# Performance work log

Hardware: AMD Instinct MI355X
Metric: run time of the kernel (lower is better)

Reference implementation:

```python
import jax, jax.numpy as jnp
import numpy as np

B, NB, S, D = 4096, 16, 256, 1024


def setup_inputs() -> dict:
    key = jax.random.key(0)
    k = jax.random.split(key, 6)
    sc_in = 1.0 / np.sqrt(D)
    sc_out = 1.0 / np.sqrt(S)
    return {
        "x": jax.random.normal(k[0], (B, D), dtype=jnp.float32),
        "y_index": jax.random.randint(k[1], (B, 1), 0, NB, dtype=jnp.int64),
        "W_in": jax.random.uniform(k[2], (NB, S, D), jnp.float32, -sc_in, sc_in),
        "b_in": jax.random.uniform(k[3], (NB, S), jnp.float32, -sc_in, sc_in),
        "W_out": jax.random.uniform(k[4], (NB, D, S), jnp.float32, -sc_out, sc_out),
        "b_out": jax.random.uniform(k[5], (NB, D), jnp.float32, -sc_out, sc_out),
    }


def reference(x, y_index, W_in, b_in, W_out, b_out):
    # h: [B, D] -> relu applied before every branch's fc_in (as in torch source)
    h = jax.nn.relu(x)
    # hiddens for all branches: [B, NB, S]
    hid = jnp.einsum("bd,nsd->bns", h, W_in) + b_in[None, :, :]
    # branch outputs stacked: [B, NB, D]
    outs = jnp.einsum("bns,nds->bnd", hid, W_out) + b_out[None, :, :]
    # gather selected branch per token: [B, D]
    sel = jnp.take_along_axis(outs, y_index[:, :, None], axis=1)[:, 0, :]
    return x + sel
```

## Files before the change

### kernel.cpp

```cpp
#include <hip/hip_runtime.h>


typedef unsigned short u16;
typedef short bf16x8 __attribute__((ext_vector_type(8)));
typedef float f32x4 __attribute__((ext_vector_type(4)));

#define MFMA16 __builtin_amdgcn_mfma_f32_16x16x32_bf16

constexpr int B_TOK = 4096;
constexpr int NB = 16;
constexpr int S_DIM = 256;
constexpr int D_DIM = 1024;
constexpr int BM = 64;
constexpr int PAD_ROWS = B_TOK + NB * BM;
constexpr int NTILES = PAD_ROWS / BM;

__device__ __forceinline__ unsigned short f2bf(float f) {
    unsigned u = __builtin_bit_cast(unsigned, f);
    u += 0x7fffu + ((u >> 16) & 1u);
    return (unsigned short)(u >> 16);
}
__device__ __forceinline__ unsigned pack2(float a, float b) {
    return (unsigned)f2bf(a) | ((unsigned)f2bf(b) << 16);
}
__device__ __forceinline__ void gload_lds16(const void* g, void* l) {
    __builtin_amdgcn_global_load_lds(
        (const __attribute__((address_space(1))) void*)g,
        (__attribute__((address_space(3))) void*)l, 16, 0, 0);
}
__device__ __forceinline__ void publish() {
    asm volatile("s_waitcnt vmcnt(0)" ::: "memory");
    __syncthreads();
}

__global__ __launch_bounds__(256) void prep_kernel(
    const float* __restrict__ Wi_f, const float* __restrict__ Wo_f,
    u16* __restrict__ Wi, u16* __restrict__ Wo,
    const int* __restrict__ y, int* __restrict__ perm, int* __restrict__ tileBranch) {
    const int t = threadIdx.x;
    if (blockIdx.x == 0) {
        __shared__ int hist[NB];
        __shared__ int aoff[NB + 1];
        __shared__ int cursor[NB];
        if (t < NB) hist[t] = 0;
        __syncthreads();
        for (int i = t; i < B_TOK; i += 256) atomicAdd(&hist[y[i]], 1);
        __syncthreads();
        if (t == 0) {
            int off = 0;
            for (int n = 0; n < NB; ++n) {
                aoff[n] = off;
                cursor[n] = off;
                off += ((hist[n] + BM - 1) / BM) * BM;
            }
            aoff[NB] = off;
        }
        __syncthreads();
        for (int i = t; i < NTILES; i += 256) {
            int rb = i * BM, br = -1;
            for (int n = 0; n < NB; ++n)
                if (rb >= aoff[n] && rb < aoff[n + 1]) br = n;
            tileBranch[i] = br;
        }
        for (int i = t; i < PAD_ROWS; i += 256) perm[i] = -1;
        __syncthreads();
        for (int i = t; i < B_TOK; i += 256) {
            int pos = atomicAdd(&cursor[y[i]], 1);
            perm[pos] = i;
        }
        return;
    }
    int i = (blockIdx.x - 1) * 256 + t;
    const float* src;
    u16* dst;
    int j;
    if (i < 524288) { src = Wi_f; dst = Wi; j = i; }
    else            { src = Wo_f; dst = Wo; j = i - 524288; }
    const float4* p = (const float4*)src + (size_t)j * 2;
    float4 v0 = p[0], v1 = p[1];
    uint4 o;
    o.x = pack2(v0.x, v0.y);
    o.y = pack2(v0.z, v0.w);
    o.z = pack2(v1.x, v1.y);
    o.w = pack2(v1.z, v1.w);
    ((uint4*)dst)[j] = o;
}

__global__ __launch_bounds__(256) void gemm1_kernel(
    const float* __restrict__ x, const u16* __restrict__ Wi,
    const float* __restrict__ b_in, const int* __restrict__ tileBranch,
    const int* __restrict__ perm, u16* __restrict__ Hp) {
    const int branch = tileBranch[blockIdx.y];
    if (branch < 0) return;
    const int rowBase = blockIdx.y * BM;
    const int colBase = blockIdx.x * 64;

    __shared__ u16 sA[2][64 * 64];
    __shared__ u16 sB[2][64 * 64];

    const int t = threadIdx.x;
    const int ar = t >> 2;
    const int acg = t & 3;
    const int tok = perm[rowBase + ar];
    const float* aSrc = (tok >= 0) ? (x + (size_t)tok * D_DIM + acg * 16) : x;
    const int abyte0 = (ar * 128 + acg * 32) ^ ((ar & 7) << 4);
    const int abyte1 = abyte0 ^ 16;

    const u16* Bb = Wi + (size_t)branch * S_DIM * D_DIM + (size_t)colBase * D_DIM;

    const int lane = t & 63;
    const int wid = t >> 6;
    const int wm = (wid >> 1) * 32;
    const int wn = (wid & 1) * 32;
    const int fr = lane & 15;
    const int kc = (lane >> 4) << 3;

    f32x4 acc[2][2] = {};

    auto stageB = [&](int buf, int k0) {
#pragma unroll
        for (int i = 0; i < 2; ++i) {
            const int L = i * 4096 + t * 16;
            const int row = L >> 7;
            const int sunit = ((L >> 4) & 7) ^ (row & 7);
            gload_lds16((const char*)Bb + (size_t)row * (D_DIM * 2) + k0 * 2 + sunit * 16,
                        (char*)sB[buf] + L);
        }
    };
    auto packWriteA = [&](int buf, float4 v0, float4 v1, float4 v2, float4 v3) {
        uint4 w0, w1;
        if (tok >= 0) {
            w0.x = pack2(fmaxf(v0.x, 0.f), fmaxf(v0.y, 0.f));
            w0.y = pack2(fmaxf(v0.z, 0.f), fmaxf(v0.w, 0.f));
            w0.z = pack2(fmaxf(v1.x, 0.f), fmaxf(v1.y, 0.f));
            w0.w = pack2(fmaxf(v1.z, 0.f), fmaxf(v1.w, 0.f));
            w1.x = pack2(fmaxf(v2.x, 0.f), fmaxf(v2.y, 0.f));
            w1.y = pack2(fmaxf(v2.z, 0.f), fmaxf(v2.w, 0.f));
            w1.z = pack2(fmaxf(v3.x, 0.f), fmaxf(v3.y, 0.f));
            w1.w = pack2(fmaxf(v3.z, 0.f), fmaxf(v3.w, 0.f));
        } else {
            w0 = make_uint4(0, 0, 0, 0);
            w1 = make_uint4(0, 0, 0, 0);
        }
        *(uint4*)((char*)sA[buf] + abyte0) = w0;
        *(uint4*)((char*)sA[buf] + abyte1) = w1;
    };

    float4 v0, v1, v2, v3;
    {
        const float4* p = (const float4*)aSrc;
        v0 = p[0]; v1 = p[1]; v2 = p[2]; v3 = p[3];
    }
    stageB(0, 0);
    packWriteA(0, v0, v1, v2, v3);
    publish();

    for (int kt = 0; kt < 16; ++kt) {
        const int cur = kt & 1;
        if (kt < 15) {
            const int k0n = (kt + 1) << 6;
            stageB(cur ^ 1, k0n);
            const float4* p = (const float4*)(aSrc + k0n);
            v0 = p[0]; v1 = p[1]; v2 = p[2]; v3 = p[3];
        }
#pragma unroll
        for (int kk = 0; kk < 2; ++kk) {
            const int kcol = kc + kk * 32;
            const int ra0 = wm + fr, ra1 = wm + 16 + fr;
            const int rb0 = wn + fr, rb1 = wn + 16 + fr;
            bf16x8 a0 = *(const bf16x8*)&sA[cur][(ra0 * 64 + kcol) ^ ((ra0 & 7) << 3)];
            bf16x8 a1 = *(const bf16x8*)&sA[cur][(ra1 * 64 + kcol) ^ ((ra1 & 7) << 3)];
            bf16x8 b0 = *(const bf16x8*)&sB[cur][(rb0 * 64 + kcol) ^ ((rb0 & 7) << 3)];
            bf16x8 b1 = *(const bf16x8*)&sB[cur][(rb1 * 64 + kcol) ^ ((rb1 & 7) << 3)];
            acc[0][0] = MFMA16(a0, b0, acc[0][0], 0, 0, 0);
            acc[0][1] = MFMA16(a0, b1, acc[0][1], 0, 0, 0);
            acc[1][0] = MFMA16(a1, b0, acc[1][0], 0, 0, 0);
            acc[1][1] = MFMA16(a1, b1, acc[1][1], 0, 0, 0);
        }
        if (kt < 15) packWriteA(cur ^ 1, v0, v1, v2, v3);
        publish();
    }

    const int r0 = (lane >> 4) * 4;
#pragma unroll
    for (int m = 0; m < 2; ++m) {
        const int prow0 = rowBase + wm + m * 16 + r0;
#pragma unroll
        for (int n = 0; n < 2; ++n) {
            const int col = colBase + wn + n * 16 + fr;
            const float bv = b_in[branch * S_DIM + col];
#pragma unroll
            for (int r = 0; r < 4; ++r)
                Hp[(size_t)(prow0 + r) * S_DIM + col] = f2bf(acc[m][n][r] + bv);
        }
    }
}

__global__ __launch_bounds__(256) void gemm2_kernel(
    const u16* __restrict__ Hp, const u16* __restrict__ Wo,
    const float* __restrict__ b_out, const int* __restrict__ tileBranch,
    const int* __restrict__ perm, const float* __restrict__ x,
    float* __restrict__ out) {
    const int branch = tileBranch[blockIdx.y];
    if (branch < 0) return;
    const int rowBase = blockIdx.y * BM;
    const int colBase = blockIdx.x * 128;

    __shared__ __align__(16) char smem[49152];
    u16* sA0 = (u16*)smem;
    u16* sA1 = (u16*)(smem + 8192);
    u16* sB0 = (u16*)(smem + 16384);
    u16* sB1 = (u16*)(smem + 32768);

    const int t = threadIdx.x;
    const u16* Ab = Hp + (size_t)rowBase * S_DIM;
    const u16* Bb = Wo + (size_t)branch * D_DIM * S_DIM + (size_t)colBase * S_DIM;

    const int lane = t & 63;
    const int wid = t >> 6;
    const int wm = (wid >> 1) * 32;
    const int wn = (wid & 1) * 64;
    const int fr = lane & 15;
    const int kc = (lane >> 4) << 3;

    f32x4 acc[2][4] = {};

    auto stage = [&](u16* dA, u16* dB, int k0) {
#pragma unroll
        for (int i = 0; i < 2; ++i) {
            const int L = i * 4096 + t * 16;
            const int row = L >> 7;
            const int sunit = ((L >> 4) & 7) ^ (row & 7);
            gload_lds16((const char*)Ab + (size_t)row * (S_DIM * 2) + k0 * 2 + sunit * 16,
                        (char*)dA + L);
        }
#pragma unroll
        for (int i = 0; i < 4; ++i) {
            const int L = i * 4096 + t * 16;
            const int row = L >> 7;
            const int sunit = ((L >> 4) & 7) ^ (row & 7);
            gload_lds16((const char*)Bb + (size_t)row * (S_DIM * 2) + k0 * 2 + sunit * 16,
                        (char*)dB + L);
        }
    };
    auto compute = [&](const u16* cA, const u16* cB) {
#pragma unroll
        for (int kk = 0; kk < 2; ++kk) {
            const int kcol = kc + kk * 32;
            const int ra0 = wm + fr, ra1 = wm + 16 + fr;
            bf16x8 a0 = *(const bf16x8*)&cA[(ra0 * 64 + kcol) ^ ((ra0 & 7) << 3)];
            bf16x8 a1 = *(const bf16x8*)&cA[(ra1 * 64 + kcol) ^ ((ra1 & 7) << 3)];
            bf16x8 b[4];
#pragma unroll
            for (int n = 0; n < 4; ++n) {
                const int rb = wn + n * 16 + fr;
                b[n] = *(const bf16x8*)&cB[(rb * 64 + kcol) ^ ((rb & 7) << 3)];
            }
#pragma unroll
            for (int n = 0; n < 4; ++n) {
                acc[0][n] = MFMA16(a0, b[n], acc[0][n], 0, 0, 0);
                acc[1][n] = MFMA16(a1, b[n], acc[1][n], 0, 0, 0);
            }
        }
    };

    stage(sA0, sB0, 0);
    publish();
#pragma unroll
    for (int kt = 0; kt < 4; ++kt) {
        const bool even = (kt & 1) == 0;
        if (kt < 3) stage(even ? sA1 : sA0, even ? sB1 : sB0, (kt + 1) << 6);
        compute(even ? sA0 : sA1, even ? sB0 : sB1);
        publish();
    }

    float* bo = (float*)smem;
    const int r0 = (lane >> 4) * 4;
#pragma unroll
    for (int m = 0; m < 2; ++m)
#pragma unroll
        for (int n = 0; n < 4; ++n)
#pragma unroll
            for (int r = 0; r < 4; ++r)
                bo[(wm + m * 16 + r0 + r) * 132 + wn + n * 16 + fr] = acc[m][n][r];
    __syncthreads();

    const int brow = t >> 2;
    const int q4 = (t & 3) * 4;
    const int tok2 = perm[rowBase + brow];
    if (tok2 >= 0) {
        const size_t gbase = (size_t)tok2 * D_DIM + colBase;
        const float* xr = x + gbase;
        float* orow = out + gbase;
        const float* br = b_out + (size_t)branch * D_DIM + colBase;
#pragma unroll
        for (int j = 0; j < 8; ++j) {
            const int c = q4 + j * 16;
            float4 xv = *(const float4*)&xr[c];
            float4 bv = *(const float4*)&br[c];
            float4 hv = *(const float4*)&bo[brow * 132 + c];
            float4 s;
            s.x = xv.x + bv.x + hv.x;
            s.y = xv.y + bv.y + hv.y;
            s.z = xv.z + bv.z + hv.z;
            s.w = xv.w + bv.w + hv.w;
            *(float4*)&orow[c] = s;
        }
    }
}

extern "C" void kernel_launch(void* const* d_in, const int* in_sizes, int n_in,
                              void* d_out, int out_size, void* d_ws, size_t ws_size,
                              hipStream_t stream) {
    const float* x     = (const float*)d_in[0];
    const int*   y     = (const int*)d_in[1];
    const float* W_in  = (const float*)d_in[2];
    const float* b_in  = (const float*)d_in[3];
    const float* W_out = (const float*)d_in[4];
    const float* b_out = (const float*)d_in[5];
    float* out = (float*)d_out;

    char* ws = (char*)d_ws;
    u16* Wi = (u16*)(ws);
    u16* Wo = (u16*)(ws + 8388608);
    u16* Hp = (u16*)(ws + 16777216);
    int* perm = (int*)(ws + 19398656);
    int* tileBranch = (int*)(ws + 19419136);

    prep_kernel<<<4097, 256, 0, stream>>>(W_in, W_out, Wi, Wo, y, perm, tileBranch);

    gemm1_kernel<<<dim3(S_DIM / 64, NTILES), 256, 0, stream>>>(
        x, Wi, b_in, tileBranch, perm, Hp);

    gemm2_kernel<<<dim3(D_DIM / 128, NTILES), 256, 0, stream>>>(
        Hp, Wo, b_out, tileBranch, perm, x, out);
}
```

Measured before the change: 55.24 us.

## Fuse weight fp32-to-bf16 conversion into GEMM tile loads, drop prep pass

```diff
diff --git a/kernel.cpp b/kernel.cpp
--- a/kernel.cpp
+++ b/kernel.cpp
@@ -33,61 +33,42 @@
     __syncthreads();
 }
 
-__global__ __launch_bounds__(256) void prep_kernel(
-    const float* __restrict__ Wi_f, const float* __restrict__ Wo_f,
-    u16* __restrict__ Wi, u16* __restrict__ Wo,
+__global__ __launch_bounds__(256) void setup_kernel(
     const int* __restrict__ y, int* __restrict__ perm, int* __restrict__ tileBranch) {
+    __shared__ int hist[NB];
+    __shared__ int aoff[NB + 1];
+    __shared__ int cursor[NB];
     const int t = threadIdx.x;
-    if (blockIdx.x == 0) {
-        __shared__ int hist[NB];
-        __shared__ int aoff[NB + 1];
-        __shared__ int cursor[NB];
-        if (t < NB) hist[t] = 0;
-        __syncthreads();
-        for (int i = t; i < B_TOK; i += 256) atomicAdd(&hist[y[i]], 1);
-        __syncthreads();
-        if (t == 0) {
-            int off = 0;
-            for (int n = 0; n < NB; ++n) {
-                aoff[n] = off;
-                cursor[n] = off;
-                off += ((hist[n] + BM - 1) / BM) * BM;
-            }
-            aoff[NB] = off;
-        }
-        __syncthreads();
-        for (int i = t; i < NTILES; i += 256) {
-            int rb = i * BM, br = -1;
-            for (int n = 0; n < NB; ++n)
-                if (rb >= aoff[n] && rb < aoff[n + 1]) br = n;
-            tileBranch[i] = br;
-        }
-        for (int i = t; i < PAD_ROWS; i += 256) perm[i] = -1;
-        __syncthreads();
-        for (int i = t; i < B_TOK; i += 256) {
-            int pos = atomicAdd(&cursor[y[i]], 1);
-            perm[pos] = i;
-        }
-        return;
-    }
-    int i = (blockIdx.x - 1) * 256 + t;
-    const float* src;
-    u16* dst;
-    int j;
-    if (i < 524288) { src = Wi_f; dst = Wi; j = i; }
-    else            { src = Wo_f; dst = Wo; j = i - 524288; }
-    const float4* p = (const float4*)src + (size_t)j * 2;
-    float4 v0 = p[0], v1 = p[1];
-    uint4 o;
-    o.x = pack2(v0.x, v0.y);
-    o.y = pack2(v0.z, v0.w);
-    o.z = pack2(v1.x, v1.y);
-    o.w = pack2(v1.z, v1.w);
-    ((uint4*)dst)[j] = o;
+    if (t < NB) hist[t] = 0;
+    __syncthreads();
+    for (int i = t; i < B_TOK; i += 256) atomicAdd(&hist[y[i]], 1);
+    __syncthreads();
+    if (t == 0) {
+        int off = 0;
+        for (int n = 0; n < NB; ++n) {
+            aoff[n] = off;
+            cursor[n] = off;
+            off += ((hist[n] + BM - 1) / BM) * BM;
+        }
+        aoff[NB] = off;
+    }
+    __syncthreads();
+    for (int i = t; i < NTILES; i += 256) {
+        int rb = i * BM, br = -1;
+        for (int n = 0; n < NB; ++n)
+            if (rb >= aoff[n] && rb < aoff[n + 1]) br = n;
+        tileBranch[i] = br;
+    }
+    for (int i = t; i < PAD_ROWS; i += 256) perm[i] = -1;
+    __syncthreads();
+    for (int i = t; i < B_TOK; i += 256) {
+        int pos = atomicAdd(&cursor[y[i]], 1);
+        perm[pos] = i;
+    }
 }
 
 __global__ __launch_bounds__(256) void gemm1_kernel(
-    const float* __restrict__ x, const u16* __restrict__ Wi,
+    const float* __restrict__ x, const float* __restrict__ Wi_f,
     const float* __restrict__ b_in, const int* __restrict__ tileBranch,
     const int* __restrict__ perm, u16* __restrict__ Hp) {
     const int branch = tileBranch[blockIdx.y];
@@ -99,14 +80,13 @@
     __shared__ u16 sB[2][64 * 64];
 
     const int t = threadIdx.x;
-    const int ar = t >> 2;
-    const int acg = t & 3;
-    const int tok = perm[rowBase + ar];
-    const float* aSrc = (tok >= 0) ? (x + (size_t)tok * D_DIM + acg * 16) : x;
-    const int abyte0 = (ar * 128 + acg * 32) ^ ((ar & 7) << 4);
-    const int abyte1 = abyte0 ^ 16;
-
-    const u16* Bb = Wi + (size_t)branch * S_DIM * D_DIM + (size_t)colBase * D_DIM;
+    const int sr = t >> 2;
+    const int scg = t & 3;
+    const int tok = perm[rowBase + sr];
+    const float* aSrc = (tok >= 0) ? (x + (size_t)tok * D_DIM + scg * 16) : x;
+    const float* bSrc = Wi_f + ((size_t)branch * S_DIM + colBase + sr) * D_DIM + scg * 16;
+    const int sbyte0 = (sr * 128 + scg * 32) ^ ((sr & 7) << 4);
+    const int sbyte1 = sbyte0 ^ 16;
 
     const int lane = t & 63;
     const int wid = t >> 6;
@@ -117,52 +97,50 @@
 
     f32x4 acc[2][2] = {};
 
-    auto stageB = [&](int buf, int k0) {
-#pragma unroll
-        for (int i = 0; i < 2; ++i) {
-            const int L = i * 4096 + t * 16;
-            const int row = L >> 7;
-            const int sunit = ((L >> 4) & 7) ^ (row & 7);
-            gload_lds16((const char*)Bb + (size_t)row * (D_DIM * 2) + k0 * 2 + sunit * 16,
-                        (char*)sB[buf] + L);
-        }
-    };
-    auto packWriteA = [&](int buf, float4 v0, float4 v1, float4 v2, float4 v3) {
-        uint4 w0, w1;
+    float4 av0, av1, av2, av3, bv0, bv1, bv2, bv3;
+    auto loadRegs = [&](int k0) {
+        const float4* pa = (const float4*)(aSrc + k0);
+        const float4* pb = (const float4*)(bSrc + k0);
+        av0 = pa[0]; av1 = pa[1]; av2 = pa[2]; av3 = pa[3];
+        bv0 = pb[0]; bv1 = pb[1]; bv2 = pb[2]; bv3 = pb[3];
+    };
+    auto packWrite = [&](int buf) {
+        uint4 wa0, wa1;
         if (tok >= 0) {
-            w0.x = pack2(fmaxf(v0.x, 0.f), fmaxf(v0.y, 0.f));
-            w0.y = pack2(fmaxf(v0.z, 0.f), fmaxf(v0.w, 0.f));
-            w0.z = pack2(fmaxf(v1.x, 0.f), fmaxf(v1.y, 0.f));
-            w0.w = pack2(fmaxf(v1.z, 0.f), fmaxf(v1.w, 0.f));
-            w1.x = pack2(fmaxf(v2.x, 0.f), fmaxf(v2.y, 0.f));
-            w1.y = pack2(fmaxf(v2.z, 0.f), fmaxf(v2.w, 0.f));
-            w1.z = pack2(fmaxf(v3.x, 0.f), fmaxf(v3.y, 0.f));
-            w1.w = pack2(fmaxf(v3.z, 0.f), fmaxf(v3.w, 0.f));
+            wa0.x = pack2(fmaxf(av0.x, 0.f), fmaxf(av0.y, 0.f));
+            wa0.y = pack2(fmaxf(av0.z, 0.f), fmaxf(av0.w, 0.f));
+            wa0.z = pack2(fmaxf(av1.x, 0.f), fmaxf(av1.y, 0.f));
+            wa0.w = pack2(fmaxf(av1.z, 0.f), fmaxf(av1.w, 0.f));
+            wa1.x = pack2(fmaxf(av2.x, 0.f), fmaxf(av2.y, 0.f));
+            wa1.y = pack2(fmaxf(av2.z, 0.f), fmaxf(av2.w, 0.f));
+            wa1.z = pack2(fmaxf(av3.x, 0.f), fmaxf(av3.y, 0.f));
+            wa1.w = pack2(fmaxf(av3.z, 0.f), fmaxf(av3.w, 0.f));
         } else {
-            w0 = make_uint4(0, 0, 0, 0);
-            w1 = make_uint4(0, 0, 0, 0);
-        }
-        *(uint4*)((char*)sA[buf] + abyte0) = w0;
-        *(uint4*)((char*)sA[buf] + abyte1) = w1;
-    };
-
-    float4 v0, v1, v2, v3;
-    {
-        const float4* p = (const float4*)aSrc;
-        v0 = p[0]; v1 = p[1]; v2 = p[2]; v3 = p[3];
-    }
-    stageB(0, 0);
-    packWriteA(0, v0, v1, v2, v3);
-    publish();
+            wa0 = make_uint4(0, 0, 0, 0);
+            wa1 = make_uint4(0, 0, 0, 0);
+        }
+        *(uint4*)((char*)sA[buf] + sbyte0) = wa0;
+        *(uint4*)((char*)sA[buf] + sbyte1) = wa1;
+        uint4 wb0, wb1;
+        wb0.x = pack2(bv0.x, bv0.y);
+        wb0.y = pack2(bv0.z, bv0.w);
+        wb0.z = pack2(bv1.x, bv1.y);
+        wb0.w = pack2(bv1.z, bv1.w);
+        wb1.x = pack2(bv2.x, bv2.y);
+        wb1.y = pack2(bv2.z, bv2.w);
+        wb1.z = pack2(bv3.x, bv3.y);
+        wb1.w = pack2(bv3.z, bv3.w);
+        *(uint4*)((char*)sB[buf] + sbyte0) = wb0;
+        *(uint4*)((char*)sB[buf] + sbyte1) = wb1;
+    };
+
+    loadRegs(0);
+    packWrite(0);
+    __syncthreads();
 
     for (int kt = 0; kt < 16; ++kt) {
         const int cur = kt & 1;
-        if (kt < 15) {
-            const int k0n = (kt + 1) << 6;
-            stageB(cur ^ 1, k0n);
-            const float4* p = (const float4*)(aSrc + k0n);
-            v0 = p[0]; v1 = p[1]; v2 = p[2]; v3 = p[3];
-        }
+        if (kt < 15) loadRegs((kt + 1) << 6);
 #pragma unroll
         for (int kk = 0; kk < 2; ++kk) {
             const int kcol = kc + kk * 32;
@@ -177,8 +155,8 @@
             acc[1][0] = MFMA16(a1, b0, acc[1][0], 0, 0, 0);
             acc[1][1] = MFMA16(a1, b1, acc[1][1], 0, 0, 0);
         }
-        if (kt < 15) packWriteA(cur ^ 1, v0, v1, v2, v3);
-        publish();
+        if (kt < 15) packWrite(cur ^ 1);
+        __syncthreads();
     }
 
     const int r0 = (lane >> 4) * 4;
@@ -188,16 +166,16 @@
 #pragma unroll
         for (int n = 0; n < 2; ++n) {
             const int col = colBase + wn + n * 16 + fr;
-            const float bv = b_in[branch * S_DIM + col];
+            const float bvs = b_in[branch * S_DIM + col];
 #pragma unroll
             for (int r = 0; r < 4; ++r)
-                Hp[(size_t)(prow0 + r) * S_DIM + col] = f2bf(acc[m][n][r] + bv);
+                Hp[(size_t)(prow0 + r) * S_DIM + col] = f2bf(acc[m][n][r] + bvs);
         }
     }
 }
 
 __global__ __launch_bounds__(256) void gemm2_kernel(
-    const u16* __restrict__ Hp, const u16* __restrict__ Wo,
+    const u16* __restrict__ Hp, const float* __restrict__ Wo_f,
     const float* __restrict__ b_out, const int* __restrict__ tileBranch,
     const int* __restrict__ perm, const float* __restrict__ x,
     float* __restrict__ out) {
@@ -214,7 +192,12 @@
 
     const int t = threadIdx.x;
     const u16* Ab = Hp + (size_t)rowBase * S_DIM;
-    const u16* Bb = Wo + (size_t)branch * D_DIM * S_DIM + (size_t)colBase * S_DIM;
+
+    const int brow = t >> 1;
+    const int bhalf = t & 1;
+    const float* bSrc = Wo_f + ((size_t)branch * D_DIM + colBase + brow) * S_DIM + bhalf * 32;
+    const int bsw = (brow & 7) << 4;
+    const int bbase = brow * 128 + bhalf * 64;
 
     const int lane = t & 63;
     const int wid = t >> 6;
@@ -225,7 +208,24 @@
 
     f32x4 acc[2][4] = {};
 
-    auto stage = [&](u16* dA, u16* dB, int k0) {
+    float4 bv[8];
+    auto loadB = [&](int k0) {
+        const float4* p = (const float4*)(bSrc + k0);
+#pragma unroll
+        for (int q = 0; q < 8; ++q) bv[q] = p[q];
+    };
+    auto writeB = [&](u16* dB) {
+#pragma unroll
+        for (int q = 0; q < 4; ++q) {
+            uint4 w;
+            w.x = pack2(bv[2 * q].x, bv[2 * q].y);
+            w.y = pack2(bv[2 * q].z, bv[2 * q].w);
+            w.z = pack2(bv[2 * q + 1].x, bv[2 * q + 1].y);
+            w.w = pack2(bv[2 * q + 1].z, bv[2 * q + 1].w);
+            *(uint4*)((char*)dB + ((bbase + q * 16) ^ bsw)) = w;
+        }
+    };
+    auto stageA = [&](u16* dA, int k0) {
 #pragma unroll
         for (int i = 0; i < 2; ++i) {
             const int L = i * 4096 + t * 16;
@@ -234,14 +234,6 @@
             gload_lds16((const char*)Ab + (size_t)row * (S_DIM * 2) + k0 * 2 + sunit * 16,
                         (char*)dA + L);
         }
-#pragma unroll
-        for (int i = 0; i < 4; ++i) {
-            const int L = i * 4096 + t * 16;
-            const int row = L >> 7;
-            const int sunit = ((L >> 4) & 7) ^ (row & 7);
-            gload_lds16((const char*)Bb + (size_t)row * (S_DIM * 2) + k0 * 2 + sunit * 16,
-                        (char*)dB + L);
-        }
     };
     auto compute = [&](const u16* cA, const u16* cB) {
 #pragma unroll
@@ -264,13 +256,23 @@
         }
     };
 
-    stage(sA0, sB0, 0);
+    stageA(sA0, 0);
+    loadB(0);
+    writeB(sB0);
     publish();
 #pragma unroll
     for (int kt = 0; kt < 4; ++kt) {
         const bool even = (kt & 1) == 0;
-        if (kt < 3) stage(even ? sA1 : sA0, even ? sB1 : sB0, (kt + 1) << 6);
-        compute(even ? sA0 : sA1, even ? sB0 : sB1);
+        u16* cA = even ? sA0 : sA1;
+        u16* cB = even ? sB0 : sB1;
+        u16* nA = even ? sA1 : sA0;
+        u16* nB = even ? sB1 : sB0;
+        if (kt < 3) {
+            stageA(nA, (kt + 1) << 6);
+            loadB((kt + 1) << 6);
+        }
+        compute(cA, cB);
+        if (kt < 3) writeB(nB);
         publish();
     }
 
@@ -285,9 +287,9 @@
                 bo[(wm + m * 16 + r0 + r) * 132 + wn + n * 16 + fr] = acc[m][n][r];
     __syncthreads();
 
-    const int brow = t >> 2;
+    const int erow = t >> 2;
     const int q4 = (t & 3) * 4;
-    const int tok2 = perm[rowBase + brow];
+    const int tok2 = perm[rowBase + erow];
     if (tok2 >= 0) {
         const size_t gbase = (size_t)tok2 * D_DIM + colBase;
         const float* xr = x + gbase;
@@ -297,13 +299,13 @@
         for (int j = 0; j < 8; ++j) {
             const int c = q4 + j * 16;
             float4 xv = *(const float4*)&xr[c];
-            float4 bv = *(const float4*)&br[c];
-            float4 hv = *(const float4*)&bo[brow * 132 + c];
+            float4 bvv = *(const float4*)&br[c];
+            float4 hv = *(const float4*)&bo[erow * 132 + c];
             float4 s;
-            s.x = xv.x + bv.x + hv.x;
-            s.y = xv.y + bv.y + hv.y;
-            s.z = xv.z + bv.z + hv.z;
-            s.w = xv.w + bv.w + hv.w;
+            s.x = xv.x + bvv.x + hv.x;
+            s.y = xv.y + bvv.y + hv.y;
+            s.z = xv.z + bvv.z + hv.z;
+            s.w = xv.w + bvv.w + hv.w;
             *(float4*)&orow[c] = s;
         }
     }
@@ -321,17 +323,15 @@
     float* out = (float*)d_out;
 
     char* ws = (char*)d_ws;
-    u16* Wi = (u16*)(ws);
-    u16* Wo = (u16*)(ws + 8388608);
-    u16* Hp = (u16*)(ws + 16777216);
-    int* perm = (int*)(ws + 19398656);
-    int* tileBranch = (int*)(ws + 19419136);
-
-    prep_kernel<<<4097, 256, 0, stream>>>(W_in, W_out, Wi, Wo, y, perm, tileBranch);
+    u16* Hp = (u16*)(ws);
+    int* perm = (int*)(ws + 2621440);
+    int* tileBranch = (int*)(ws + 2641920);
+
+    setup_kernel<<<1, 256, 0, stream>>>(y, perm, tileBranch);
 
     gemm1_kernel<<<dim3(S_DIM / 64, NTILES), 256, 0, stream>>>(
-        x, Wi, b_in, tileBranch, perm, Hp);
+        x, W_in, b_in, tileBranch, perm, Hp);
 
     gemm2_kernel<<<dim3(D_DIM / 128, NTILES), 256, 0, stream>>>(
-        Hp, Wo, b_out, tileBranch, perm, x, out);
-}
+        Hp, W_out, b_out, tileBranch, perm, x, out);
+}
```

Result: slower. 60.57 us (+9.7%).

## Move W_out bf16 cast from prep kernel into gemm1 tail

Applied to the files above, without the earlier changes.

```diff
diff --git a/kernel.cpp b/kernel.cpp
--- a/kernel.cpp
+++ b/kernel.cpp
@@ -14,6 +14,7 @@
 constexpr int BM = 64;
 constexpr int PAD_ROWS = B_TOK + NB * BM;
 constexpr int NTILES = PAD_ROWS / BM;
+constexpr int W_ITEMS = NB * S_DIM * D_DIM / 8;
 
 __device__ __forceinline__ unsigned short f2bf(float f) {
     unsigned u = __builtin_bit_cast(unsigned, f);
@@ -32,10 +33,20 @@
     asm volatile("s_waitcnt vmcnt(0)" ::: "memory");
     __syncthreads();
 }
+__device__ __forceinline__ void cast8(const float* __restrict__ src,
+                                      u16* __restrict__ dst, int j) {
+    const float4* p = (const float4*)src + (size_t)j * 2;
+    float4 v0 = p[0], v1 = p[1];
+    uint4 o;
+    o.x = pack2(v0.x, v0.y);
+    o.y = pack2(v0.z, v0.w);
+    o.z = pack2(v1.x, v1.y);
+    o.w = pack2(v1.z, v1.w);
+    ((uint4*)dst)[j] = o;
+}
 
 __global__ __launch_bounds__(256) void prep_kernel(
-    const float* __restrict__ Wi_f, const float* __restrict__ Wo_f,
-    u16* __restrict__ Wi, u16* __restrict__ Wo,
+    const float* __restrict__ Wi_f, u16* __restrict__ Wi,
     const int* __restrict__ y, int* __restrict__ perm, int* __restrict__ tileBranch) {
     const int t = threadIdx.x;
     if (blockIdx.x == 0) {
@@ -70,130 +81,123 @@
         }
         return;
     }
-    int i = (blockIdx.x - 1) * 256 + t;
-    const float* src;
-    u16* dst;
-    int j;
-    if (i < 524288) { src = Wi_f; dst = Wi; j = i; }
-    else            { src = Wo_f; dst = Wo; j = i - 524288; }
-    const float4* p = (const float4*)src + (size_t)j * 2;
-    float4 v0 = p[0], v1 = p[1];
-    uint4 o;
-    o.x = pack2(v0.x, v0.y);
-    o.y = pack2(v0.z, v0.w);
-    o.z = pack2(v1.x, v1.y);
-    o.w = pack2(v1.z, v1.w);
-    ((uint4*)dst)[j] = o;
+    cast8(Wi_f, Wi, (blockIdx.x - 1) * 256 + t);
 }
 
 __global__ __launch_bounds__(256) void gemm1_kernel(
     const float* __restrict__ x, const u16* __restrict__ Wi,
     const float* __restrict__ b_in, const int* __restrict__ tileBranch,
-    const int* __restrict__ perm, u16* __restrict__ Hp) {
+    const int* __restrict__ perm, u16* __restrict__ Hp,
+    const float* __restrict__ Wo_f, u16* __restrict__ Wo) {
     const int branch = tileBranch[blockIdx.y];
-    if (branch < 0) return;
-    const int rowBase = blockIdx.y * BM;
-    const int colBase = blockIdx.x * 64;
-
-    __shared__ u16 sA[2][64 * 64];
-    __shared__ u16 sB[2][64 * 64];
-
     const int t = threadIdx.x;
-    const int ar = t >> 2;
-    const int acg = t & 3;
-    const int tok = perm[rowBase + ar];
-    const float* aSrc = (tok >= 0) ? (x + (size_t)tok * D_DIM + acg * 16) : x;
-    const int abyte0 = (ar * 128 + acg * 32) ^ ((ar & 7) << 4);
-    const int abyte1 = abyte0 ^ 16;
-
-    const u16* Bb = Wi + (size_t)branch * S_DIM * D_DIM + (size_t)colBase * D_DIM;
-
-    const int lane = t & 63;
-    const int wid = t >> 6;
-    const int wm = (wid >> 1) * 32;
-    const int wn = (wid & 1) * 32;
-    const int fr = lane & 15;
-    const int kc = (lane >> 4) << 3;
-
-    f32x4 acc[2][2] = {};
-
-    auto stageB = [&](int buf, int k0) {
-#pragma unroll
-        for (int i = 0; i < 2; ++i) {
-            const int L = i * 4096 + t * 16;
-            const int row = L >> 7;
-            const int sunit = ((L >> 4) & 7) ^ (row & 7);
-            gload_lds16((const char*)Bb + (size_t)row * (D_DIM * 2) + k0 * 2 + sunit * 16,
-                        (char*)sB[buf] + L);
-        }
-    };
-    auto packWriteA = [&](int buf, float4 v0, float4 v1, float4 v2, float4 v3) {
-        uint4 w0, w1;
-        if (tok >= 0) {
-            w0.x = pack2(fmaxf(v0.x, 0.f), fmaxf(v0.y, 0.f));
-            w0.y = pack2(fmaxf(v0.z, 0.f), fmaxf(v0.w, 0.f));
-            w0.z = pack2(fmaxf(v1.x, 0.f), fmaxf(v1.y, 0.f));
-            w0.w = pack2(fmaxf(v1.z, 0.f), fmaxf(v1.w, 0.f));
-            w1.x = pack2(fmaxf(v2.x, 0.f), fmaxf(v2.y, 0.f));
-            w1.y = pack2(fmaxf(v2.z, 0.f), fmaxf(v2.w, 0.f));
-            w1.z = pack2(fmaxf(v3.x, 0.f), fmaxf(v3.y, 0.f));
-            w1.w = pack2(fmaxf(v3.z, 0.f), fmaxf(v3.w, 0.f));
-        } else {
-            w0 = make_uint4(0, 0, 0, 0);
-            w1 = make_uint4(0, 0, 0, 0);
-        }
-        *(uint4*)((char*)sA[buf] + abyte0) = w0;
-        *(uint4*)((char*)sA[buf] + abyte1) = w1;
-    };
-
-    float4 v0, v1, v2, v3;
-    {
-        const float4* p = (const float4*)aSrc;
-        v0 = p[0]; v1 = p[1]; v2 = p[2]; v3 = p[3];
+
+    if (branch >= 0) {
+        const int rowBase = blockIdx.y * BM;
+        const int colBase = blockIdx.x * 64;
+
+        __shared__ u16 sA[2][64 * 64];
+        __shared__ u16 sB[2][64 * 64];
+
+        const int sr = t >> 2;
+        const int scg = t & 3;
+        const int tok = perm[rowBase + sr];
+        const float* aSrc = (tok >= 0) ? (x + (size_t)tok * D_DIM + scg * 16) : x;
+        const int sbyte0 = (sr * 128 + scg * 32) ^ ((sr & 7) << 4);
+        const int sbyte1 = sbyte0 ^ 16;
+
+        const u16* Bb = Wi + (size_t)branch * S_DIM * D_DIM + (size_t)colBase * D_DIM;
+
+        const int lane = t & 63;
+        const int wid = t >> 6;
+        const int wm = (wid >> 1) * 32;
+        const int wn = (wid & 1) * 32;
+        const int fr = lane & 15;
+        const int kc = (lane >> 4) << 3;
+
+        f32x4 acc[2][2] = {};
+        float4 av0, av1, av2, av3;
+
+        auto loadA = [&](int k0) {
+            const float4* pa = (const float4*)(aSrc + k0);
+            av0 = pa[0]; av1 = pa[1]; av2 = pa[2]; av3 = pa[3];
+        };
+        auto stageB = [&](int buf, int k0) {
+#pragma unroll
+            for (int i = 0; i < 2; ++i) {
+                const int L = i * 4096 + t * 16;
+                const int row = L >> 7;
+                const int sunit = ((L >> 4) & 7) ^ (row & 7);
+                gload_lds16((const char*)Bb + (size_t)row * (D_DIM * 2) + k0 * 2 + sunit * 16,
+                            (char*)sB[buf] + L);
+            }
+        };
+        auto packWriteA = [&](int buf) {
+            uint4 w0, w1;
+            if (tok >= 0) {
+                w0.x = pack2(fmaxf(av0.x, 0.f), fmaxf(av0.y, 0.f));
+                w0.y = pack2(fmaxf(av0.z, 0.f), fmaxf(av0.w, 0.f));
+                w0.z = pack2(fmaxf(av1.x, 0.f), fmaxf(av1.y, 0.f));
+                w0.w = pack2(fmaxf(av1.z, 0.f), fmaxf(av1.w, 0.f));
+                w1.x = pack2(fmaxf(av2.x, 0.f), fmaxf(av2.y, 0.f));
+                w1.y = pack2(fmaxf(av2.z, 0.f), fmaxf(av2.w, 0.f));
+                w1.z = pack2(fmaxf(av3.x, 0.f), fmaxf(av3.y, 0.f));
+                w1.w = pack2(fmaxf(av3.z, 0.f), fmaxf(av3.w, 0.f));
+            } else {
+                w0 = make_uint4(0, 0, 0, 0);
+                w1 = make_uint4(0, 0, 0, 0);
+            }
+            *(uint4*)((char*)sA[buf] + sbyte0) = w0;
+            *(uint4*)((char*)sA[buf] + sbyte1) = w1;
+        };
+
+        loadA(0);
+        stageB(0, 0);
+        packWriteA(0);
+        publish();
+
+        for (int kt = 0; kt < 16; ++kt) {
+            const int cur = kt & 1;
+            if (kt < 15) {
+                stageB(cur ^ 1, (kt + 1) << 6);
+                loadA((kt + 1) << 6);
+            }
+#pragma unroll
+            for (int kk = 0; kk < 2; ++kk) {
+                const int kcol = kc + kk * 32;
+                const int ra0 = wm + fr, ra1 = wm + 16 + fr;
+                const int rb0 = wn + fr, rb1 = wn + 16 + fr;
+                bf16x8 a0 = *(const bf16x8*)&sA[cur][(ra0 * 64 + kcol) ^ ((ra0 & 7) << 3)];
+                bf16x8 a1 = *(const bf16x8*)&sA[cur][(ra1 * 64 + kcol) ^ ((ra1 & 7) << 3)];
+                bf16x8 b0 = *(const bf16x8*)&sB[cur][(rb0 * 64 + kcol) ^ ((rb0 & 7) << 3)];
+                bf16x8 b1 = *(const bf16x8*)&sB[cur][(rb1 * 64 + kcol) ^ ((rb1 & 7) << 3)];
+                acc[0][0] = MFMA16(a0, b0, acc[0][0], 0, 0, 0);
+                acc[0][1] = MFMA16(a0, b1, acc[0][1], 0, 0, 0);
+                acc[1][0] = MFMA16(a1, b0, acc[1][0], 0, 0, 0);
+                acc[1][1] = MFMA16(a1, b1, acc[1][1], 0, 0, 0);
+            }
+            if (kt < 15) packWriteA(cur ^ 1);
+            publish();
+        }
+
+        const int r0 = (lane >> 4) * 4;
+#pragma unroll
+        for (int m = 0; m < 2; ++m) {
+            const int prow0 = rowBase + wm + m * 16 + r0;
+#pragma unroll
+            for (int n = 0; n < 2; ++n) {
+                const int col = colBase + wn + n * 16 + fr;
+                const float bvs = b_in[branch * S_DIM + col];
+#pragma unroll
+                for (int r = 0; r < 4; ++r)
+                    Hp[(size_t)(prow0 + r) * S_DIM + col] = f2bf(acc[m][n][r] + bvs);
+            }
+        }
     }
-    stageB(0, 0);
-    packWriteA(0, v0, v1, v2, v3);
-    publish();
-
-    for (int kt = 0; kt < 16; ++kt) {
-        const int cur = kt & 1;
-        if (kt < 15) {
-            const int k0n = (kt + 1) << 6;
-            stageB(cur ^ 1, k0n);
-            const float4* p = (const float4*)(aSrc + k0n);
-            v0 = p[0]; v1 = p[1]; v2 = p[2]; v3 = p[3];
-        }
-#pragma unroll
-        for (int kk = 0; kk < 2; ++kk) {
-            const int kcol = kc + kk * 32;
-            const int ra0 = wm + fr, ra1 = wm + 16 + fr;
-            const int rb0 = wn + fr, rb1 = wn + 16 + fr;
-            bf16x8 a0 = *(const bf16x8*)&sA[cur][(ra0 * 64 + kcol) ^ ((ra0 & 7) << 3)];
-            bf16x8 a1 = *(const bf16x8*)&sA[cur][(ra1 * 64 + kcol) ^ ((ra1 & 7) << 3)];
-            bf16x8 b0 = *(const bf16x8*)&sB[cur][(rb0 * 64 + kcol) ^ ((rb0 & 7) << 3)];
-            bf16x8 b1 = *(const bf16x8*)&sB[cur][(rb1 * 64 + kcol) ^ ((rb1 & 7) << 3)];
-            acc[0][0] = MFMA16(a0, b0, acc[0][0], 0, 0, 0);
-            acc[0][1] = MFMA16(a0, b1, acc[0][1], 0, 0, 0);
-            acc[1][0] = MFMA16(a1, b0, acc[1][0], 0, 0, 0);
-            acc[1][1] = MFMA16(a1, b1, acc[1][1], 0, 0, 0);
-        }
-        if (kt < 15) packWriteA(cur ^ 1, v0, v1, v2, v3);
-        publish();
-    }
-
-    const int r0 = (lane >> 4) * 4;
-#pragma unroll
-    for (int m = 0; m < 2; ++m) {
-        const int prow0 = rowBase + wm + m * 16 + r0;
-#pragma unroll
-        for (int n = 0; n < 2; ++n) {
-            const int col = colBase + wn + n * 16 + fr;
-            const float bv = b_in[branch * S_DIM + col];
-#pragma unroll
-            for (int r = 0; r < 4; ++r)
-                Hp[(size_t)(prow0 + r) * S_DIM + col] = f2bf(acc[m][n][r] + bv);
-        }
-    }
+
+    const int bid = blockIdx.y * 4 + blockIdx.x;
+    for (int j = bid * 256 + t; j < W_ITEMS; j += 4 * NTILES * 256)
+        cast8(Wo_f, Wo, j);
 }
 
 __global__ __launch_bounds__(256) void gemm2_kernel(
@@ -269,8 +273,12 @@
 #pragma unroll
     for (int kt = 0; kt < 4; ++kt) {
         const bool even = (kt & 1) == 0;
-        if (kt < 3) stage(even ? sA1 : sA0, even ? sB1 : sB0, (kt + 1) << 6);
-        compute(even ? sA0 : sA1, even ? sB0 : sB1);
+        u16* cA = even ? sA0 : sA1;
+        u16* cB = even ? sB0 : sB1;
+        u16* nA = even ? sA1 : sA0;
+        u16* nB = even ? sB1 : sB0;
+        if (kt < 3) stage(nA, nB, (kt + 1) << 6);
+        compute(cA, cB);
         publish();
     }
 
@@ -285,9 +293,9 @@
                 bo[(wm + m * 16 + r0 + r) * 132 + wn + n * 16 + fr] = acc[m][n][r];
     __syncthreads();
 
-    const int brow = t >> 2;
+    const int erow = t >> 2;
     const int q4 = (t & 3) * 4;
-    const int tok2 = perm[rowBase + brow];
+    const int tok2 = perm[rowBase + erow];
     if (tok2 >= 0) {
         const size_t gbase = (size_t)tok2 * D_DIM + colBase;
         const float* xr = x + gbase;
@@ -297,13 +305,13 @@
         for (int j = 0; j < 8; ++j) {
             const int c = q4 + j * 16;
             float4 xv = *(const float4*)&xr[c];
-            float4 bv = *(const float4*)&br[c];
-            float4 hv = *(const float4*)&bo[brow * 132 + c];
+            float4 bvv = *(const float4*)&br[c];
+            float4 hv = *(const float4*)&bo[erow * 132 + c];
             float4 s;
-            s.x = xv.x + bv.x + hv.x;
-            s.y = xv.y + bv.y + hv.y;
-            s.z = xv.z + bv.z + hv.z;
-            s.w = xv.w + bv.w + hv.w;
+            s.x = xv.x + bvv.x + hv.x;
+            s.y = xv.y + bvv.y + hv.y;
+            s.z = xv.z + bvv.z + hv.z;
+            s.w = xv.w + bvv.w + hv.w;
             *(float4*)&orow[c] = s;
         }
     }
@@ -327,10 +335,10 @@
     int* perm = (int*)(ws + 19398656);
     int* tileBranch = (int*)(ws + 19419136);
 
-    prep_kernel<<<4097, 256, 0, stream>>>(W_in, W_out, Wi, Wo, y, perm, tileBranch);
+    prep_kernel<<<2049, 256, 0, stream>>>(W_in, Wi, y, perm, tileBranch);
 
     gemm1_kernel<<<dim3(S_DIM / 64, NTILES), 256, 0, stream>>>(
-        x, Wi, b_in, tileBranch, perm, Hp);
+        x, Wi, b_in, tileBranch, perm, Hp, W_out, Wo);
 
     gemm2_kernel<<<dim3(D_DIM / 128, NTILES), 256, 0, stream>>>(
         Hp, Wo, b_out, tileBranch, perm, x, out);
```

Measured after the change: 56.21 us. About the same (+1.8%).
